# Kernel optimization log

Measured on AMD Instinct MI355X. Metric: run time of the kernel, lower is better.

## Reference

```python
import jax, jax.numpy as jnp
import numpy as np

B, F, H, L, K = 16384, 1024, 1024, 256, 7

def _lin(key, fi, fo, lead=()):
    k1, k2 = jax.random.split(key)
    s = 1.0 / np.sqrt(fi)
    W = jax.random.uniform(k1, lead + (fi, fo), jnp.float32, -s, s)
    b = jax.random.uniform(k2, lead + (fo,), jnp.float32, -s, s)
    return W, b

def setup_inputs() -> dict:
    ks = jax.random.split(jax.random.key(0), 16)
    x = jax.random.normal(ks[0], (B, F), jnp.float32)
    t = jax.random.randint(ks[1], (B,), 0, K, jnp.int32)
    y = jax.random.normal(ks[2], (B,), jnp.float32)
    d = jax.random.normal(ks[3], (B,), jnp.float32)
    tw0, tb0 = _lin(ks[4], F, L)
    tw1, tb1 = _lin(ks[5], L, L)
    tw2, tb2 = _lin(ks[6], L, K)
    yw0, yb0 = _lin(ks[7], F, H)
    yw1, yb1 = _lin(ks[8], H, H)
    yhW, yhb = _lin(ks[9], H, 2, (K,))
    dw0, db0 = _lin(ks[10], F, H)
    dw1, db1 = _lin(ks[11], H, H)
    dhW, dhb = _lin(ks[12], H, 2, (K,))
    zw0, zb0 = _lin(ks[13], F + 2, H)
    zw1, zb1 = _lin(ks[14], H, H)
    zhW, zhb = _lin(ks[15], H, 2 * L, (K,))
    return dict(x=x, t=t, y=y, d=d, tw0=tw0, tb0=tb0, tw1=tw1, tb1=tb1, tw2=tw2, tb2=tb2,
                yw0=yw0, yb0=yb0, yw1=yw1, yb1=yb1, yhW=yhW, yhb=yhb,
                dw0=dw0, db0=db0, dw1=dw1, db1=db1, dhW=dhW, dhb=dhb,
                zw0=zw0, zb0=zb0, zw1=zw1, zb1=zb1, zhW=zhW, zhb=zhb)

def _mlp2(x, w0, b0, w1, b1):
    # FullyConnected([in, H, H], final_activation=ELU)
    return jax.nn.elu(jax.nn.elu(x @ w0 + b0) @ w1 + b1)

def _select(hidden, t, hW, hb):
    # dense compute of all K treatment heads, then per-row gather by t
    all_out = jnp.einsum('bh,khd->bkd', hidden, hW) + hb  # [B, K, D]
    return jnp.take_along_axis(all_out, t[:, None, None], axis=1)[:, 0]

def _normal_head(sel):
    # pyro NormalNet head on a scalar outcome
    loc = jnp.clip(sel[:, 0:1], -1e6, 1e6)
    scale = jnp.minimum(jax.nn.softplus(sel[:, 1:2]) + 1e-3, 1e6)
    return loc, scale

def _diagnormal_head(sel):
    loc = jnp.clip(sel[:, :L], -100.0, 100.0)
    scale = jnp.minimum(jax.nn.softplus(sel[:, L:]) + 0.001, 100.0)
    return loc, scale

def reference(x, t, y, d, tw0, tb0, tw1, tb1, tw2, tb2,
              yw0, yb0, yw1, yb1, yhW, yhb,
              dw0, db0, dw1, db1, dhW, dhb,
              zw0, zb0, zw1, zb1, zhW, zhb):
    # t_nn: MultinormNet, ELU final activation then clamp(-10, 10)
    t_logits = jnp.clip(jax.nn.elu(_mlp2(x, tw0, tb0, tw1, tb1) @ tw2 + tb2), -10.0, 10.0)
    # y_dist(t, x)
    hy = _mlp2(x, yw0, yb0, yw1, yb1)
    y_loc, y_scale = _normal_head(_select(hy, t, yhW, yhb))
    # d_dist(t, x)
    hd = _mlp2(x, dw0, db0, dw1, db1)
    d_loc, d_scale = _normal_head(_select(hd, t, dhW, dhb))
    # z_dist(y, d, t, x): hidden from cat([y, d, x])
    hz = _mlp2(jnp.concatenate([y[:, None], d[:, None], x], axis=-1), zw0, zb0, zw1, zb1)
    z_loc, z_scale = _diagnormal_head(_select(hz, t, zhW, zhb))
    # [B, K + 4 + 2L]
    return jnp.concatenate([t_logits, y_loc, y_scale, d_loc, d_scale, z_loc, z_scale], axis=-1)
```

## Files before the change

kernel.cpp:

```cpp
#include <hip/hip_runtime.h>
#include <hip/hip_bf16.h>
#include <cstdint>
#include <cstddef>

typedef __hip_bfloat16 bf16;
typedef __bf16 bf16x8 __attribute__((ext_vector_type(8)));
typedef float f32x4 __attribute__((ext_vector_type(4)));

#define DEVFN static __device__ __forceinline__

DEVFN void async16(const void* g, void* l) {
  __builtin_amdgcn_global_load_lds(
      (const __attribute__((address_space(1))) uint32_t*)g,
      (__attribute__((address_space(3))) uint32_t*)l, 16, 0, 0);
}

DEVFN float eluf(float v) { return v > 0.f ? v : expm1f(v); }
DEVFN float softplusf(float x) {
  return x > 0.f ? x + log1pf(expf(-x)) : log1pf(expf(x));
}

template <int NAH, int NBH, int NFB>
DEVFN void kloop32(const bf16* (&gA)[NAH], const bf16* (&gB)[NBH], bf16* As,
                   bf16* Bs, int tid, const bf16* aBase, const bf16* bBase,
                   int colsel, f32x4 (&acc)[4][NFB], int kiters) {
  for (int kt = 0; kt < kiters; ++kt) {
#pragma unroll
    for (int c = 0; c < NAH; ++c) async16(gA[c], As + c * 2048 + tid * 8);
#pragma unroll
    for (int c = 0; c < NBH; ++c) async16(gB[c], Bs + c * 2048 + tid * 8);
#pragma unroll
    for (int c = 0; c < NAH; ++c) gA[c] += 32;
#pragma unroll
    for (int c = 0; c < NBH; ++c) gB[c] += 32;
    __syncthreads();
    bf16x8 af[4], bfv[NFB];
#pragma unroll
    for (int r = 0; r < 4; ++r) af[r] = *(const bf16x8*)(aBase + r * 512 + colsel);
#pragma unroll
    for (int c = 0; c < NFB; ++c) bfv[c] = *(const bf16x8*)(bBase + c * 512 + colsel);
#pragma unroll
    for (int r = 0; r < 4; ++r)
#pragma unroll
      for (int c = 0; c < NFB; ++c)
        acc[r][c] = __builtin_amdgcn_mfma_f32_16x16x32_bf16(af[r], bfv[c], acc[r][c], 0, 0, 0);
    __syncthreads();
  }
}

DEVFN int swz_scol(int tid) { return (((tid & 3) ^ ((tid >> 3) & 3)) * 8); }
DEVFN int swz_colsel(int quad, int l15) { return ((quad ^ ((l15 >> 1) & 3)) * 8); }

DEVFN void transpose_tile(const float* src, bf16* dst, int R, int C, int bx, int by) {
  __shared__ float tile[32][33];
  const int c0 = bx * 32, r0 = by * 32;
  const int tx = threadIdx.x & 31, ty = threadIdx.x >> 5;
#pragma unroll
  for (int rr = ty; rr < 32; rr += 8)
    tile[rr][tx] = src[(size_t)(r0 + rr) * C + c0 + tx];
  __syncthreads();
#pragma unroll
  for (int rr = ty; rr < 32; rr += 8)
    dst[(size_t)(c0 + rr) * R + r0 + tx] = __float2bfloat16(tile[tx][rr]);
}

__global__ __launch_bounds__(256) void prep_all_k(
    const float* __restrict__ x, bf16* __restrict__ xb,
    const float* __restrict__ yw0, const float* __restrict__ dw0,
    const float* __restrict__ zw0, const float* __restrict__ tw0,
    bf16* __restrict__ BtL1,
    const float* __restrict__ yw1, const float* __restrict__ dw1,
    const float* __restrict__ zw1, bf16* __restrict__ BtL2,
    const float* __restrict__ tw1, bf16* __restrict__ tw1t,
    const float* __restrict__ zhW, bf16* __restrict__ zhWt,
    const float* __restrict__ yb0, const float* __restrict__ db0,
    const float* __restrict__ zb0, const float* __restrict__ tb0,
    const float* __restrict__ yb1, const float* __restrict__ db1,
    const float* __restrict__ zb1,
    float* __restrict__ biasAll, float* __restrict__ r0All,
    float* __restrict__ r1All, float* __restrict__ biasL2,
    const int* __restrict__ t, int* __restrict__ cnt, int* __restrict__ seg,
    int* __restrict__ rank, int* __restrict__ sids) {
  int l = blockIdx.x;
  if (l < 8192) {
    size_t i = ((size_t)l * 256 + threadIdx.x) * 8;
    float4 v0 = *(const float4*)(x + i);
    float4 v1 = *(const float4*)(x + i + 4);
    union { bf16 h[8]; uint4 u; } o;
    o.h[0] = __float2bfloat16(v0.x); o.h[1] = __float2bfloat16(v0.y);
    o.h[2] = __float2bfloat16(v0.z); o.h[3] = __float2bfloat16(v0.w);
    o.h[4] = __float2bfloat16(v1.x); o.h[5] = __float2bfloat16(v1.y);
    o.h[6] = __float2bfloat16(v1.z); o.h[7] = __float2bfloat16(v1.w);
    *(uint4*)(xb + i) = o.u;
    return;
  }
  l -= 8192;
  if (l < 4096) {
    int z = l >> 10, rem = l & 1023, bx = rem & 31, by = rem >> 5;
    const float* src = (z == 0) ? yw0 : (z == 1) ? dw0 : (z == 2) ? zw0 + 2048 : tw0;
    int C = (z == 3) ? 256 : 1024;
    if (bx * 32 < C)
      transpose_tile(src, BtL1 + (size_t)z * 1024 * 1024, 1024, C, bx, by);
    return;
  }
  l -= 4096;
  if (l < 3072) {
    int z = l >> 10, rem = l & 1023, bx = rem & 31, by = rem >> 5;
    const float* src = (z == 0) ? yw1 : (z == 1) ? dw1 : zw1;
    transpose_tile(src, BtL2 + (size_t)z * 1024 * 1024, 1024, 1024, bx, by);
    return;
  }
  l -= 3072;
  if (l < 64) {
    transpose_tile(tw1, tw1t, 256, 256, l & 7, l >> 3);
    return;
  }
  l -= 64;
  if (l < 3584) {
    int z = l >> 9, rem = l & 511, bx = rem & 15, by = rem >> 4;
    transpose_tile(zhW + (size_t)z * 1024 * 512, zhWt + (size_t)z * 512 * 1024,
                   1024, 512, bx, by);
    return;
  }
  l -= 3584;
  if (l < 13) {
    int i = l * 256 + threadIdx.x;
    if (i >= 3328) return;
    float b;
    if (i < 1024) b = yb0[i];
    else if (i < 2048) b = db0[i - 1024];
    else if (i < 3072) b = zb0[i - 2048];
    else b = tb0[i - 3072];
    biasAll[i] = b;
    bool inz = (i >= 2048 && i < 3072);
    r0All[i] = inz ? zw0[i - 2048] : 0.f;
    r1All[i] = inz ? zw0[1024 + (i - 2048)] : 0.f;
    if (i < 3072)
      biasL2[i] = (i < 1024) ? yb1[i] : (i < 2048) ? db1[i - 1024] : zb1[i - 2048];
    return;
  }
  {
    __shared__ int h[8], sseg[8];
    const int tid = threadIdx.x;
    if (tid < 8) h[tid] = 0;
    __syncthreads();
    const int base = tid * 64;
    int lc[7] = {0, 0, 0, 0, 0, 0, 0};
    for (int i = 0; i < 64; ++i) lc[t[base + i]]++;
    int myoff[7];
#pragma unroll
    for (int k = 0; k < 7; ++k) myoff[k] = atomicAdd(&h[k], lc[k]);
    __syncthreads();
    if (tid == 0) {
      int s = 0;
      for (int k = 0; k < 7; ++k) { sseg[k] = s; s += h[k]; }
      sseg[7] = s;
    }
    __syncthreads();
    if (tid < 7) { cnt[tid] = h[tid]; seg[tid] = sseg[tid]; }
    if (tid == 7) seg[7] = sseg[7];
    int cur[7];
#pragma unroll
    for (int k = 0; k < 7; ++k) cur[k] = sseg[k] + myoff[k];
    for (int i = 0; i < 64; ++i) {
      int b = base + i, k = t[b];
      int r = cur[k]++;
      rank[b] = r;
      sids[r] = b;
    }
  }
}

__global__ __launch_bounds__(256) void gemm_l1_k(
    const bf16* __restrict__ A, const bf16* __restrict__ Bt,
    const float* __restrict__ biasAll, const float* __restrict__ r0All,
    const float* __restrict__ r1All, const float* __restrict__ yv,
    const float* __restrict__ dv, bf16* __restrict__ a1y,
    bf16* __restrict__ a1d, bf16* __restrict__ a1z, bf16* __restrict__ ht1) {
  __shared__ bf16 As[128 * 32];
  __shared__ bf16 Bs[128 * 32];
  const int tid = threadIdx.x, lane = tid & 63, wid = tid >> 6;
  const int wm = wid >> 1, wn = wid & 1, quad = lane >> 4, l15 = lane & 15;
  const int id = blockIdx.x;
  const int xcd = id & 7, lid = id >> 3;
  const int pass = lid / 208, rem = lid - pass * 208;
  const int mt = xcd * 16 + pass * 8 + (rem & 7), nt = rem >> 3;
  const int bm0 = mt * 128, bn0 = nt * 128;
  const int sr = tid >> 2, scol = swz_scol(tid);
  const bf16* gA[2];
  const bf16* gB[2];
#pragma unroll
  for (int c = 0; c < 2; ++c) {
    gA[c] = A + (size_t)(bm0 + c * 64 + sr) * 1024 + scol;
    gB[c] = Bt + (size_t)(bn0 + c * 64 + sr) * 1024 + scol;
  }
  const bf16* aBase = &As[(wm * 64 + l15) * 32];
  const bf16* bBase = &Bs[(wn * 64 + l15) * 32];
  const int colsel = swz_colsel(quad, l15);
  f32x4 acc[4][4] = {};
  kloop32<2, 2, 4>(gA, gB, As, Bs, tid, aBase, bBase, colsel, acc, 32);

  const int g = nt >> 3;
  bf16* dst = (g == 0) ? a1y : (g == 1) ? a1d : (g == 2) ? a1z : ht1;
  const int ldc = (g == 3) ? 256 : 1024;
  const int colb = bn0 - g * 1024;
  float bv[4], z0[4], z1[4];
#pragma unroll
  for (int c = 0; c < 4; ++c) {
    int gn = bn0 + wn * 64 + c * 16 + l15;
    bv[c] = biasAll[gn]; z0[c] = r0All[gn]; z1[c] = r1All[gn];
  }
#pragma unroll
  for (int r = 0; r < 4; ++r) {
#pragma unroll
    for (int q = 0; q < 4; ++q) {
      int gm = bm0 + wm * 64 + r * 16 + quad * 4 + q;
      float yy = yv[gm], dd = dv[gm];
#pragma unroll
      for (int c = 0; c < 4; ++c) {
        float v = acc[r][c][q] + bv[c] + yy * z0[c] + dd * z1[c];
        dst[(size_t)gm * ldc + colb + wn * 64 + c * 16 + l15] = __float2bfloat16(eluf(v));
      }
    }
  }
}

__global__ __launch_bounds__(256) void gemm_l2t_k(
    const bf16* __restrict__ a1y, const bf16* __restrict__ a1d,
    const bf16* __restrict__ a1z, const bf16* __restrict__ ht1,
    const bf16* __restrict__ BtL2, const bf16* __restrict__ tw1t,
    const float* __restrict__ biasL2, const float* __restrict__ tb1,
    bf16* __restrict__ hyd, bf16* __restrict__ hzg, bf16* __restrict__ ht2,
    const int* __restrict__ rank) {
  __shared__ bf16 As[128 * 32];
  __shared__ bf16 Bs[128 * 32];
  const int tid = threadIdx.x, lane = tid & 63, wid = tid >> 6;
  const int wm = wid >> 1, wn = wid & 1, quad = lane >> 4, l15 = lane & 15;
  const int id = blockIdx.x;
  int bm0, bn0, Ka, g;
  const bf16 *Aptr, *Bptr;
  if (id < 3072) {
    const int xcd = id & 7, lid = id >> 3;
    const int pass = lid / 192, rem = lid - pass * 192;
    const int mt = xcd * 16 + pass * 8 + (rem & 7), nt = rem >> 3;
    bm0 = mt * 128; bn0 = nt * 128; Ka = 1024;
    g = nt >> 3;
    Aptr = (g == 0) ? a1y : (g == 1) ? a1d : a1z;
    Bptr = BtL2;
  } else {
    const int local = id - 3072;
    bm0 = (local >> 1) * 128; bn0 = (local & 1) * 128; Ka = 256;
    g = 3; Aptr = ht1; Bptr = tw1t;
  }
  const int sr = tid >> 2, scol = swz_scol(tid);
  const bf16* gA[2];
  const bf16* gB[2];
#pragma unroll
  for (int c = 0; c < 2; ++c) {
    gA[c] = Aptr + (size_t)(bm0 + c * 64 + sr) * Ka + scol;
    gB[c] = Bptr + (size_t)(bn0 + c * 64 + sr) * Ka + scol;
  }
  const bf16* aBase = &As[(wm * 64 + l15) * 32];
  const bf16* bBase = &Bs[(wn * 64 + l15) * 32];
  const int colsel = swz_colsel(quad, l15);
  f32x4 acc[4][4] = {};
  kloop32<2, 2, 4>(gA, gB, As, Bs, tid, aBase, bBase, colsel, acc, Ka >> 5);

  const float* bias = (g == 3) ? tb1 : biasL2;
  float bv[4];
#pragma unroll
  for (int c = 0; c < 4; ++c) bv[c] = bias[bn0 + wn * 64 + c * 16 + l15];
#pragma unroll
  for (int r = 0; r < 4; ++r) {
#pragma unroll
    for (int q = 0; q < 4; ++q) {
      int gm = bm0 + wm * 64 + r * 16 + quad * 4 + q;
      bf16* dst; size_t rowoff;
      if (g == 2) { dst = hzg; rowoff = (size_t)rank[gm] * 1024 + (size_t)(bn0 - 2048); }
      else if (g == 3) { dst = ht2; rowoff = (size_t)gm * 256 + bn0; }
      else { dst = hyd; rowoff = (size_t)gm * 2048 + bn0; }
#pragma unroll
      for (int c = 0; c < 4; ++c) {
        float v = acc[r][c][q] + bv[c];
        dst[rowoff + wn * 64 + c * 16 + l15] = __float2bfloat16(eluf(v));
      }
    }
  }
}

#define ZMT 28
#define ZB (7 * ZMT * 8)
__global__ __launch_bounds__(256) void tail_k(
    const bf16* __restrict__ hzg, const bf16* __restrict__ zhWt,
    const float* __restrict__ zhb, const int* __restrict__ seg,
    const int* __restrict__ cnts, const int* __restrict__ sids,
    const bf16* __restrict__ hyd, const bf16* __restrict__ ht2,
    const int* __restrict__ t, const float* __restrict__ yhW,
    const float* __restrict__ yhb, const float* __restrict__ dhW,
    const float* __restrict__ dhb, const float* __restrict__ tw2,
    const float* __restrict__ tb2, float* __restrict__ out) {
  __shared__ bf16 As[128 * 32];
  __shared__ bf16 Bs[64 * 32];
  const int tid = threadIdx.x, lane = tid & 63, wid = tid >> 6;
  const int wv = wid, quad = lane >> 4, l15 = lane & 15;
  if (blockIdx.x < ZB) {
    const int kb = blockIdx.x / (ZMT * 8);
    const int r = blockIdx.x % (ZMT * 8);
    const int cnt = cnts[kb];
    const int bm0 = (r >> 3) * 128;
    if (bm0 >= cnt) return;
    const int n0 = (r & 7) * 64;
    const int wm = wid >> 1, wn = wid & 1;
    const int base = seg[kb];
    const int sr = tid >> 2, scol = swz_scol(tid);
    const bf16* gA[2];
    const bf16* gB[1];
#pragma unroll
    for (int c = 0; c < 2; ++c) {
      int rr = bm0 + c * 64 + sr;
      if (rr >= cnt) rr = cnt - 1;
      gA[c] = hzg + (size_t)(base + rr) * 1024 + scol;
    }
    gB[0] = zhWt + (size_t)kb * 512 * 1024 + (size_t)(n0 + sr) * 1024 + scol;
    const bf16* aBase = &As[(wm * 64 + l15) * 32];
    const bf16* bBase = &Bs[(wn * 32 + l15) * 32];
    const int colsel = swz_colsel(quad, l15);
    f32x4 acc[4][2] = {};
    kloop32<2, 1, 2>(gA, gB, As, Bs, tid, aBase, bBase, colsel, acc, 32);
    const float* bias = zhb + (size_t)kb * 512;
    float bv[2]; int gnn[2];
#pragma unroll
    for (int c = 0; c < 2; ++c) {
      gnn[c] = n0 + wn * 32 + c * 16 + l15;
      bv[c] = bias[gnn[c]];
    }
#pragma unroll
    for (int r2 = 0; r2 < 4; ++r2)
#pragma unroll
      for (int q = 0; q < 4; ++q) {
        int lm = bm0 + wm * 64 + r2 * 16 + quad * 4 + q;
        if (lm < cnt) {
          int gm = sids[base + lm];
          size_t ob = (size_t)gm * 523 + 11;
#pragma unroll
          for (int c = 0; c < 2; ++c) {
            float v = acc[r2][c][q] + bv[c];
            int n = gnn[c];
            out[ob + n] = (n < 256) ? fminf(fmaxf(v, -100.f), 100.f)
                                    : fminf(softplusf(v) + 0.001f, 100.f);
          }
        }
      }
    return;
  }
  const int hid = blockIdx.x - ZB;
  if (hid < 4096) {
    const int b = hid * 4 + wv;
    const int tb = t[b];
    const float* yW = yhW + (size_t)tb * 2048;
    const float* dW = dhW + (size_t)tb * 2048;
    float s0 = 0.f, s1 = 0.f, s2 = 0.f, s3 = 0.f;
    for (int i = lane; i < 1024; i += 64) {
      float a = __bfloat162float(hyd[(size_t)b * 2048 + i]);
      float c = __bfloat162float(hyd[(size_t)b * 2048 + 1024 + i]);
      s0 += a * yW[2 * i]; s1 += a * yW[2 * i + 1];
      s2 += c * dW[2 * i]; s3 += c * dW[2 * i + 1];
    }
#pragma unroll
    for (int off = 32; off > 0; off >>= 1) {
      s0 += __shfl_down(s0, off); s1 += __shfl_down(s1, off);
      s2 += __shfl_down(s2, off); s3 += __shfl_down(s3, off);
    }
    if (lane == 0) {
      size_t o = (size_t)b * 523;
      out[o + 7] = fminf(fmaxf(s0 + yhb[tb * 2], -1e6f), 1e6f);
      out[o + 8] = fminf(softplusf(s1 + yhb[tb * 2 + 1]) + 1e-3f, 1e6f);
      out[o + 9] = fminf(fmaxf(s2 + dhb[tb * 2], -1e6f), 1e6f);
      out[o + 10] = fminf(softplusf(s3 + dhb[tb * 2 + 1]) + 1e-3f, 1e6f);
    }
  } else {
    const int b = (hid - 4096) * 4 + wv;
    float h[4];
#pragma unroll
    for (int j = 0; j < 4; ++j)
      h[j] = __bfloat162float(ht2[(size_t)b * 256 + lane * 4 + j]);
    float pp[7];
#pragma unroll
    for (int kk = 0; kk < 7; ++kk) {
      float s = 0.f;
#pragma unroll
      for (int j = 0; j < 4; ++j) s += h[j] * tw2[(lane * 4 + j) * 7 + kk];
      pp[kk] = s;
    }
#pragma unroll
    for (int kk = 0; kk < 7; ++kk)
#pragma unroll
      for (int off = 32; off > 0; off >>= 1) pp[kk] += __shfl_down(pp[kk], off);
    if (lane == 0) {
#pragma unroll
      for (int kk = 0; kk < 7; ++kk) {
        float v = eluf(pp[kk] + tb2[kk]);
        out[(size_t)b * 523 + kk] = fminf(fmaxf(v, -10.f), 10.f);
      }
    }
  }
}

extern "C" void kernel_launch(void* const* d_in, const int* in_sizes, int n_in,
                              void* d_out, int out_size, void* d_ws, size_t ws_size,
                              hipStream_t stream) {
  const float* x   = (const float*)d_in[0];
  const int*   t   = (const int*)d_in[1];
  const float* yv  = (const float*)d_in[2];
  const float* dv  = (const float*)d_in[3];
  const float* tw0 = (const float*)d_in[4];
  const float* tb0 = (const float*)d_in[5];
  const float* tw1 = (const float*)d_in[6];
  const float* tb1 = (const float*)d_in[7];
  const float* tw2 = (const float*)d_in[8];
  const float* tb2 = (const float*)d_in[9];
  const float* yw0 = (const float*)d_in[10];
  const float* yb0 = (const float*)d_in[11];
  const float* yw1 = (const float*)d_in[12];
  const float* yb1 = (const float*)d_in[13];
  const float* yhW = (const float*)d_in[14];
  const float* yhb = (const float*)d_in[15];
  const float* dw0 = (const float*)d_in[16];
  const float* db0 = (const float*)d_in[17];
  const float* dw1 = (const float*)d_in[18];
  const float* db1 = (const float*)d_in[19];
  const float* dhW = (const float*)d_in[20];
  const float* dhb = (const float*)d_in[21];
  const float* zw0 = (const float*)d_in[22];
  const float* zb0 = (const float*)d_in[23];
  const float* zw1 = (const float*)d_in[24];
  const float* zb1 = (const float*)d_in[25];
  const float* zhW = (const float*)d_in[26];
  const float* zhb = (const float*)d_in[27];
  float* out = (float*)d_out;

  const int B = 16384;
  char* p = (char*)d_ws;
  auto take = [&](size_t bytes) {
    char* r = p;
    p += (bytes + 255) & ~(size_t)255;
    return r;
  };
  bf16*  BtL1    = (bf16*)take((size_t)3328 * 1024 * 2);
  bf16*  BtL2    = (bf16*)take((size_t)3072 * 1024 * 2);
  bf16*  tw1t    = (bf16*)take((size_t)256 * 256 * 2);
  bf16*  zhWt    = (bf16*)take((size_t)7 * 512 * 1024 * 2);
  float* biasAll = (float*)take(3328 * 4);
  float* r0All   = (float*)take(3328 * 4);
  float* r1All   = (float*)take(3328 * 4);
  float* biasL2  = (float*)take(3072 * 4);
  int*   cnt     = (int*)take(8 * 4);
  int*   seg     = (int*)take(8 * 4);
  int*   rank    = (int*)take((size_t)B * 4);
  int*   sids    = (int*)take((size_t)B * 4);
  bf16*  xb      = (bf16*)take((size_t)B * 1024 * 2);
  bf16*  a1y     = (bf16*)take((size_t)B * 1024 * 2);
  bf16*  a1d     = (bf16*)take((size_t)B * 1024 * 2);
  bf16*  a1z     = (bf16*)take((size_t)B * 1024 * 2);
  bf16*  ht1     = (bf16*)take((size_t)B * 256 * 2);
  bf16*  hyd     = (bf16*)take((size_t)B * 2048 * 2);
  bf16*  ht2     = (bf16*)take((size_t)B * 256 * 2);
  bf16*  hzg     = xb;

  prep_all_k<<<19022, 256, 0, stream>>>(x, xb, yw0, dw0, zw0, tw0, BtL1,
                                        yw1, dw1, zw1, BtL2, tw1, tw1t, zhW, zhWt,
                                        yb0, db0, zb0, tb0, yb1, db1, zb1,
                                        biasAll, r0All, r1All, biasL2,
                                        t, cnt, seg, rank, sids);
  gemm_l1_k<<<3328, 256, 0, stream>>>(xb, BtL1, biasAll, r0All, r1All,
                                      yv, dv, a1y, a1d, a1z, ht1);
  gemm_l2t_k<<<3328, 256, 0, stream>>>(a1y, a1d, a1z, ht1, BtL2, tw1t,
                                       biasL2, tb1, hyd, hzg, ht2, rank);
  tail_k<<<ZB + 8192, 256, 0, stream>>>(hzg, zhWt, zhb, seg, cnt, sids,
                                        hyd, ht2, t, yhW, yhb, dhW, dhb,
                                        tw2, tb2, out);
}
```

Before: 661.8 us.

## Load B fragments directly from global into registers in layer-1 GEMM

Measured after the change: 786.5 us. +18.8%, slower.

```diff
diff --git a/kernel.cpp b/kernel.cpp
--- a/kernel.cpp
+++ b/kernel.cpp
@@ -178,7 +178,6 @@
     const float* __restrict__ dv, bf16* __restrict__ a1y,
     bf16* __restrict__ a1d, bf16* __restrict__ a1z, bf16* __restrict__ ht1) {
   __shared__ bf16 As[128 * 32];
-  __shared__ bf16 Bs[128 * 32];
   const int tid = threadIdx.x, lane = tid & 63, wid = tid >> 6;
   const int wm = wid >> 1, wn = wid & 1, quad = lane >> 4, l15 = lane & 15;
   const int id = blockIdx.x;
@@ -187,18 +186,33 @@
   const int mt = xcd * 16 + pass * 8 + (rem & 7), nt = rem >> 3;
   const int bm0 = mt * 128, bn0 = nt * 128;
   const int sr = tid >> 2, scol = swz_scol(tid);
-  const bf16* gA[2];
-  const bf16* gB[2];
-#pragma unroll
-  for (int c = 0; c < 2; ++c) {
-    gA[c] = A + (size_t)(bm0 + c * 64 + sr) * 1024 + scol;
-    gB[c] = Bt + (size_t)(bn0 + c * 64 + sr) * 1024 + scol;
-  }
+  const bf16* gA0 = A + (size_t)(bm0 + sr) * 1024 + scol;
+  const bf16* gA1 = A + (size_t)(bm0 + 64 + sr) * 1024 + scol;
+  const bf16* gBf[4];
+#pragma unroll
+  for (int c = 0; c < 4; ++c)
+    gBf[c] = Bt + (size_t)(bn0 + wn * 64 + c * 16 + l15) * 1024 + quad * 8;
   const bf16* aBase = &As[(wm * 64 + l15) * 32];
-  const bf16* bBase = &Bs[(wn * 64 + l15) * 32];
   const int colsel = swz_colsel(quad, l15);
   f32x4 acc[4][4] = {};
-  kloop32<2, 2, 4>(gA, gB, As, Bs, tid, aBase, bBase, colsel, acc, 32);
+  for (int kt = 0; kt < 32; ++kt) {
+    async16(gA0, As + tid * 8);
+    async16(gA1, As + 2048 + tid * 8);
+    gA0 += 32; gA1 += 32;
+    bf16x8 bfv[4];
+#pragma unroll
+    for (int c = 0; c < 4; ++c) bfv[c] = *(const bf16x8*)(gBf[c] + kt * 32);
+    __syncthreads();
+    bf16x8 af[4];
+#pragma unroll
+    for (int r = 0; r < 4; ++r) af[r] = *(const bf16x8*)(aBase + r * 512 + colsel);
+#pragma unroll
+    for (int r = 0; r < 4; ++r)
+#pragma unroll
+      for (int c = 0; c < 4; ++c)
+        acc[r][c] = __builtin_amdgcn_mfma_f32_16x16x32_bf16(af[r], bfv[c], acc[r][c], 0, 0, 0);
+    __syncthreads();
+  }
 
   const int g = nt >> 3;
   bf16* dst = (g == 0) ? a1y : (g == 1) ? a1d : (g == 2) ? a1z : ht1;
```
